# Performance work log

Measured on AMD Instinct MI355X. Metric: run time of the kernel, lower is better.

Reference implementation:

```python
import jax, jax.numpy as jnp
import numpy as np

H = 2048           # hidden size
IN_F = 64          # in_features
OUT_F = 3          # out_features
NEG_SLOPE = 0.01   # LeakyReLU default


def setup_inputs() -> dict:
    key = jax.random.key(0)
    ks = jax.random.split(key, 11)
    N = 32768
    return {
        "p": jax.random.normal(ks[0], (N, IN_F), dtype=jnp.float32),
        "init_w": jax.random.normal(ks[1], (H, IN_F), dtype=jnp.float32) * 0.05,
        "init_b": jax.random.normal(ks[2], (H,), dtype=jnp.float32) * 0.05,
        "w1": jax.random.normal(ks[3], (H, H), dtype=jnp.float32) * 0.02,
        "b1": jax.random.normal(ks[4], (H,), dtype=jnp.float32) * 0.02,
        "w2": jax.random.normal(ks[5], (H, H), dtype=jnp.float32) * 0.02,
        "b2": jax.random.normal(ks[6], (H,), dtype=jnp.float32) * 0.02,
        "w3": jax.random.normal(ks[7], (H, H), dtype=jnp.float32) * 0.02,
        "b3": jax.random.normal(ks[8], (H,), dtype=jnp.float32) * 0.02,
        "out_w": jax.random.normal(ks[9], (OUT_F, H), dtype=jnp.float32) * 0.05,
        "out_b": jax.random.normal(ks[10], (OUT_F,), dtype=jnp.float32) * 0.05,
    }


def _leaky_relu(x):
    return jnp.where(x > 0, x, NEG_SLOPE * x)


def reference(p, init_w, init_b, w1, b1, w2, b2, w3, b3, out_w, out_b):
    # eval mode: StructuredDropout with eval_size=None -> plain init linear
    flat = p.reshape(-1, p.shape[-1])                      # [N, IN_F]
    x = flat @ init_w.T + init_b                           # [N, H]
    # upper-triangular mask (in==out, backflow=0 -> diagonal=0)
    mask = jnp.triu(jnp.ones((H, H), dtype=bool))
    # hidden TriangleLinear layers; flip = (i % 2 == 1)
    for W, b, flip in ((w1, b1, False), (w2, b2, True), (w3, b3, False)):
        y = _leaky_relu(x) @ jnp.where(mask, W, 0.0).T + b  # [N, H]
        x = y[..., ::-1] if flip else y
    x = _leaky_relu(x)
    out = x @ out_w.T + out_b                              # [N, OUT_F]
    return out.reshape(p.shape[:-1] + (OUT_F,))
```

## Files before the change

kernel.cpp:

```cpp
#include <hip/hip_runtime.h>
#include <hip/hip_bf16.h>

#define NEG 0.01f

using f32x4  = __attribute__((ext_vector_type(4))) float;
using bf16x8 = __attribute__((ext_vector_type(8))) short;

__device__ __forceinline__ unsigned short f2b(float f) {
  union { float f; unsigned int u; } v; v.f = f;
  unsigned int r = (v.u + 0x7fffu + ((v.u >> 16) & 1u)) >> 16;
  return (unsigned short)r;
}
__device__ __forceinline__ float b2f(unsigned int bits) {
  union { unsigned int u; float f; } v; v.u = bits << 16;
  return v.f;
}

__device__ __forceinline__ void gload16(const unsigned short* g, unsigned short* l) {
  __builtin_amdgcn_global_load_lds(
      (const __attribute__((address_space(1))) unsigned int*)g,
      (__attribute__((address_space(3))) unsigned int*)l, 16, 0, 0);
}

__global__ void k_cvt(const float* __restrict__ in, unsigned short* __restrict__ out, int n4) {
  int i = blockIdx.x * blockDim.x + threadIdx.x;
  int stride = gridDim.x * blockDim.x;
  for (; i < n4; i += stride) {
    float4 v = reinterpret_cast<const float4*>(in)[i];
    ushort4 o;
    o.x = f2b(v.x); o.y = f2b(v.y); o.z = f2b(v.z); o.w = f2b(v.w);
    reinterpret_cast<ushort4*>(out)[i] = o;
  }
}

__global__ void k_cvt_tri(const float* __restrict__ W, unsigned short* __restrict__ out, int anti) {
  const int H = 2048;
  int i = blockIdx.x;
  const float* wr = W + (size_t)i * H;
  unsigned short* orow = out + (size_t)i * H;
  if (!anti) {
    for (int j = threadIdx.x; j < H; j += blockDim.x) {
      float v = (j >= i) ? wr[j] : 0.f;
      orow[j] = f2b(v);
    }
  } else {
    for (int k = threadIdx.x; k < H; k += blockDim.x) {
      int j = H - 1 - k;
      float v = (j >= i) ? wr[j] : 0.f;
      orow[k] = f2b(v);
    }
  }
}

__launch_bounds__(512)
__global__ void k_gemm(const unsigned short* __restrict__ A, int lda,
                       const unsigned short* __restrict__ B, int ldb,
                       const float* __restrict__ bias,
                       unsigned short* __restrict__ C, int ldc,
                       int K, int mode) {
  __shared__ unsigned short As[128 * 32];
  __shared__ unsigned short Bs[256 * 32];
  const int tid  = threadIdx.x;
  const int w    = tid >> 6;
  const int lane = tid & 63;

  const int nwg = gridDim.x;
  const int q   = nwg >> 3;
  const int L   = blockIdx.x;
  const int logical = (L & 7) * q + (L >> 3);
  const int bx = logical & 7;
  const int by = logical >> 3;
  const int brow = by * 128;
  const int bcol = bx * 256;

  int kstart = 0, kend = K;
  if (mode == 1) kstart = bcol;
  else if (mode == 2) kend = K - bcol;

  const int wm = w >> 2;
  const int wn = w & 3;
  f32x4 zero = {0.f, 0.f, 0.f, 0.f};
  f32x4 acc[4][4];
#pragma unroll
  for (int i = 0; i < 4; i++)
#pragma unroll
    for (int j = 0; j < 4; j++) acc[i][j] = zero;

  const int sr = lane >> 2;
  const int sc = (lane & 3) * 8;
  const unsigned short* Abase = A + (size_t)(brow + w * 16 + sr) * lda + sc;
  const unsigned short* Bbase = B + (size_t)(bcol + w * 16 + sr) * ldb + sc;
  unsigned short* AsW = &As[(w * 16) * 32];
  unsigned short* BsW = &Bs[(w * 16) * 32];

  const int lrow = lane & 15;
  const int lk   = (lane >> 4) * 8;

  for (int kt = kstart; kt < kend; kt += 32) {
    gload16(Abase + kt,                        AsW);
    gload16(Bbase + kt,                        BsW);
    gload16(Bbase + (size_t)128 * ldb + kt,    BsW + 128 * 32);
    __syncthreads();

    bf16x8 af[4], bfr[4];
#pragma unroll
    for (int i = 0; i < 4; i++) {
      af[i]  = *reinterpret_cast<const bf16x8*>(&As[(wm * 64 + i * 16 + lrow) * 32 + lk]);
      bfr[i] = *reinterpret_cast<const bf16x8*>(&Bs[(wn * 64 + i * 16 + lrow) * 32 + lk]);
    }
#pragma unroll
    for (int i = 0; i < 4; i++)
#pragma unroll
      for (int j = 0; j < 4; j++)
        acc[i][j] = __builtin_amdgcn_mfma_f32_16x16x32_bf16(af[i], bfr[j], acc[i][j], 0, 0, 0);
    __syncthreads();
  }

  const int orow0 = brow + wm * 64 + (lane >> 4) * 4;
  const int ocol0 = bcol + wn * 64 + (lane & 15);
#pragma unroll
  for (int j = 0; j < 4; j++) {
    int col = ocol0 + j * 16;
    float bv = bias[col];
#pragma unroll
    for (int i = 0; i < 4; i++) {
#pragma unroll
      for (int r = 0; r < 4; r++) {
        int row = orow0 + i * 16 + r;
        float v = acc[i][j][r] + bv;
        v = v > 0.f ? v : NEG * v;
        C[(size_t)row * ldc + col] = f2b(v);
      }
    }
  }
}

__global__ void k_out(const unsigned short* __restrict__ A,
                      const float* __restrict__ ow, const float* __restrict__ ob,
                      float* __restrict__ out) {
  const int H = 2048;
  int w = threadIdx.x >> 6, lane = threadIdx.x & 63;
  size_t n = (size_t)blockIdx.x * 4 + w;
  const unsigned short* a = A + n * H;
  float s0 = 0.f, s1 = 0.f, s2 = 0.f;
  for (int h0 = lane * 8; h0 < H; h0 += 512) {
    uint4 u = *reinterpret_cast<const uint4*>(&a[h0]);
    unsigned int uu[4] = {u.x, u.y, u.z, u.w};
#pragma unroll
    for (int q = 0; q < 4; q++) {
      int h = h0 + q * 2;
      float x0 = b2f(uu[q] & 0xffffu);
      float x1 = b2f(uu[q] >> 16);
      s0 += x0 * ow[h]         + x1 * ow[h + 1];
      s1 += x0 * ow[H + h]     + x1 * ow[H + h + 1];
      s2 += x0 * ow[2 * H + h] + x1 * ow[2 * H + h + 1];
    }
  }
#pragma unroll
  for (int off = 32; off > 0; off >>= 1) {
    s0 += __shfl_down(s0, off);
    s1 += __shfl_down(s1, off);
    s2 += __shfl_down(s2, off);
  }
  if (lane == 0) {
    out[n * 3 + 0] = s0 + ob[0];
    out[n * 3 + 1] = s1 + ob[1];
    out[n * 3 + 2] = s2 + ob[2];
  }
}

extern "C" void kernel_launch(void* const* d_in, const int* in_sizes, int n_in,
                              void* d_out, int out_size, void* d_ws, size_t ws_size,
                              hipStream_t stream) {
  const int N = 32768, H = 2048, INF_ = 64;
  const float* p      = (const float*)d_in[0];
  const float* init_w = (const float*)d_in[1];
  const float* init_b = (const float*)d_in[2];
  const float* w1     = (const float*)d_in[3];
  const float* b1     = (const float*)d_in[4];
  const float* w2     = (const float*)d_in[5];
  const float* b2     = (const float*)d_in[6];
  const float* w3     = (const float*)d_in[7];
  const float* b3     = (const float*)d_in[8];
  const float* ow     = (const float*)d_in[9];
  const float* ob     = (const float*)d_in[10];

  char* wsb = (char*)d_ws;
  size_t off = 0;
  auto alloc = [&](size_t bytes) -> char* {
    char* q = wsb + off;
    off += (bytes + 255) & ~(size_t)255;
    return q;
  };
  unsigned short* pb  = (unsigned short*)alloc((size_t)N * INF_ * 2);
  unsigned short* iwb = (unsigned short*)alloc((size_t)H * INF_ * 2);
  unsigned short* w1m = (unsigned short*)alloc((size_t)H * H * 2);
  unsigned short* w2m = (unsigned short*)alloc((size_t)H * H * 2);
  unsigned short* w3m = (unsigned short*)alloc((size_t)H * H * 2);

  size_t remain = (ws_size > off) ? (ws_size - off) : 0;
  long long ncll = (long long)(remain / ((size_t)H * 2 * 2));
  int Nc = (int)((ncll / 128) * 128);
  if (Nc > N) Nc = N;
  if (Nc < 128) return;

  unsigned short* bufA = (unsigned short*)(wsb + off);
  unsigned short* bufB = bufA + (size_t)Nc * H;

  k_cvt<<<2048, 256, 0, stream>>>(p, pb, N * INF_ / 4);
  k_cvt<<<32,   256, 0, stream>>>(init_w, iwb, H * INF_ / 4);
  k_cvt_tri<<<H, 256, 0, stream>>>(w1, w1m, 0);
  k_cvt_tri<<<H, 256, 0, stream>>>(w2, w2m, 0);
  k_cvt_tri<<<H, 256, 0, stream>>>(w3, w3m, 1);

  for (int n0 = 0; n0 < N; n0 += Nc) {
    int nc = (N - n0 < Nc) ? (N - n0) : Nc;
    int nblk = (H / 256) * (nc / 128);
    k_gemm<<<nblk, 512, 0, stream>>>(pb + (size_t)n0 * INF_, INF_, iwb, INF_, init_b,
                                     bufA, H, INF_, 0);
    k_gemm<<<nblk, 512, 0, stream>>>(bufA, H, w1m, H, b1, bufB, H, H, 1);
    k_gemm<<<nblk, 512, 0, stream>>>(bufB, H, w2m, H, b2, bufA, H, H, 1);
    k_gemm<<<nblk, 512, 0, stream>>>(bufA, H, w3m, H, b3, bufB, H, H, 2);
    k_out<<<nc / 4, 256, 0, stream>>>(bufB, ow, ob, (float*)d_out + (size_t)n0 * 3);
  }
}
```

Before: 859.5 us.

## Rewrite GEMM with 256x256 tiles, double-buffered LDS and swizzled layout

```diff
diff --git a/kernel.cpp b/kernel.cpp
--- a/kernel.cpp
+++ b/kernel.cpp
@@ -52,81 +52,125 @@
   }
 }
 
-__launch_bounds__(512)
-__global__ void k_gemm(const unsigned short* __restrict__ A, int lda,
-                       const unsigned short* __restrict__ B, int ldb,
-                       const float* __restrict__ bias,
-                       unsigned short* __restrict__ C, int ldc,
-                       int K, int mode) {
-  __shared__ unsigned short As[128 * 32];
-  __shared__ unsigned short Bs[256 * 32];
-  const int tid  = threadIdx.x;
-  const int w    = tid >> 6;
-  const int lane = tid & 63;
+__launch_bounds__(512, 2)
+__global__ void k_gemm8(const unsigned short* __restrict__ A, int lda,
+                        const unsigned short* __restrict__ B, int ldb,
+                        const float* __restrict__ bias,
+                        unsigned short* __restrict__ C, int ldc,
+                        int K, int mode) {
+  extern __shared__ unsigned short lds[];
+  const int tid = threadIdx.x;
+  const int w   = tid >> 6;
+  const int l   = tid & 63;
 
   const int nwg = gridDim.x;
-  const int q   = nwg >> 3;
+  const int q8  = nwg >> 3;
   const int L   = blockIdx.x;
-  const int logical = (L & 7) * q + (L >> 3);
-  const int bx = logical & 7;
+  const int logical = (L & 7) * q8 + (L >> 3);
   const int by = logical >> 3;
-  const int brow = by * 128;
+  const int bx = (logical + by) & 7;
+  const int brow = by * 256;
   const int bcol = bx * 256;
 
   int kstart = 0, kend = K;
   if (mode == 1) kstart = bcol;
   else if (mode == 2) kend = K - bcol;
+  const int nt = (kend - kstart) >> 6;
 
   const int wm = w >> 2;
   const int wn = w & 3;
-  f32x4 zero = {0.f, 0.f, 0.f, 0.f};
-  f32x4 acc[4][4];
-#pragma unroll
-  for (int i = 0; i < 4; i++)
-#pragma unroll
-    for (int j = 0; j < 4; j++) acc[i][j] = zero;
-
-  const int sr = lane >> 2;
-  const int sc = (lane & 3) * 8;
-  const unsigned short* Abase = A + (size_t)(brow + w * 16 + sr) * lda + sc;
-  const unsigned short* Bbase = B + (size_t)(bcol + w * 16 + sr) * ldb + sc;
-  unsigned short* AsW = &As[(w * 16) * 32];
-  unsigned short* BsW = &Bs[(w * 16) * 32];
-
-  const int lrow = lane & 15;
-  const int lk   = (lane >> 4) * 8;
-
-  for (int kt = kstart; kt < kend; kt += 32) {
-    gload16(Abase + kt,                        AsW);
-    gload16(Bbase + kt,                        BsW);
-    gload16(Bbase + (size_t)128 * ldb + kt,    BsW + 128 * 32);
-    __syncthreads();
-
-    bf16x8 af[4], bfr[4];
-#pragma unroll
-    for (int i = 0; i < 4; i++) {
-      af[i]  = *reinterpret_cast<const bf16x8*>(&As[(wm * 64 + i * 16 + lrow) * 32 + lk]);
-      bfr[i] = *reinterpret_cast<const bf16x8*>(&Bs[(wn * 64 + i * 16 + lrow) * 32 + lk]);
-    }
-#pragma unroll
-    for (int i = 0; i < 4; i++)
-#pragma unroll
-      for (int j = 0; j < 4; j++)
-        acc[i][j] = __builtin_amdgcn_mfma_f32_16x16x32_bf16(af[i], bfr[j], acc[i][j], 0, 0, 0);
-    __syncthreads();
-  }
-
-  const int orow0 = brow + wm * 64 + (lane >> 4) * 4;
-  const int ocol0 = bcol + wn * 64 + (lane & 15);
+
+  f32x4 acc[8][4];
+#pragma unroll
+  for (int i = 0; i < 8; i++)
+#pragma unroll
+    for (int j = 0; j < 4; j++) acc[i][j] = (f32x4){0.f, 0.f, 0.f, 0.f};
+
+  const int srow  = l >> 2;
+  const int sperm = ((l & 3) - ((l >> 3) & 3)) & 3;
+  const unsigned short* Asrc = A + (size_t)(brow + w * 16 + srow) * lda + sperm * 8;
+  const unsigned short* Bsrc = B + (size_t)(bcol + w * 16 + srow) * ldb + sperm * 8;
+  const int rdoff = (l & 15) * 64 + ((((l >> 4) + ((l >> 1) & 7)) & 3) << 4);
+
+  auto ldsAt = [&](int byteoff) -> unsigned short* {
+    return (unsigned short*)((char*)lds + byteoff);
+  };
+  auto stage_tile = [&](int tk, int bb) {
+    const int kc = kstart + (tk << 6);
+#pragma unroll
+    for (int half = 0; half < 2; half++) {
+#pragma unroll
+      for (int qq = 0; qq < 2; qq++) {
+        gload16(Asrc + (size_t)(half * 128) * lda + kc + qq * 32,
+                ldsAt(bb * 65536 + half * 16384 + (w * 2 + qq) * 1024));
+        gload16(Bsrc + (size_t)(half * 128) * ldb + kc + qq * 32,
+                ldsAt(bb * 65536 + 32768 + half * 16384 + (w * 2 + qq) * 1024));
+      }
+    }
+  };
+
+  stage_tile(0, 0);
+  if (nt > 1) stage_tile(1, 1);
+
+  const int AbaseW = wm * 16384;
+  const int BbaseW = 32768 + (wn >> 1) * 16384 + (wn & 1) * 8192;
+
+  for (int t = 0; t < nt; t++) {
+    const int bb = t & 1;
+    const int Ab = bb * 65536 + AbaseW;
+    const int Bb = bb * 65536 + BbaseW;
+    if (t + 1 < nt) asm volatile("s_waitcnt vmcnt(8)" ::: "memory");
+    else            asm volatile("s_waitcnt vmcnt(0)" ::: "memory");
+    __builtin_amdgcn_s_barrier();
+    asm volatile("" ::: "memory");
+
+    bf16x8 aR[4][2], bR[2][2];
+#pragma unroll
+    for (int Q = 0; Q < 4; Q++) {
+      const int mh = Q >> 1, nh = Q & 1;
+      if (nh == 0) {
+#pragma unroll
+        for (int ii = 0; ii < 4; ii++)
+#pragma unroll
+          for (int kk = 0; kk < 2; kk++)
+            aR[ii][kk] = *(const bf16x8*)((char*)lds + Ab + ((mh * 4 + ii) * 2 + kk) * 1024 + rdoff);
+      }
+#pragma unroll
+      for (int jj = 0; jj < 2; jj++)
+#pragma unroll
+        for (int kk = 0; kk < 2; kk++)
+          bR[jj][kk] = *(const bf16x8*)((char*)lds + Bb + ((nh * 2 + jj) * 2 + kk) * 1024 + rdoff);
+
+      __builtin_amdgcn_s_setprio(1);
+#pragma unroll
+      for (int ii = 0; ii < 4; ii++)
+#pragma unroll
+        for (int jj = 0; jj < 2; jj++) {
+          acc[mh * 4 + ii][nh * 2 + jj] = __builtin_amdgcn_mfma_f32_16x16x32_bf16(
+              aR[ii][0], bR[jj][0], acc[mh * 4 + ii][nh * 2 + jj], 0, 0, 0);
+          acc[mh * 4 + ii][nh * 2 + jj] = __builtin_amdgcn_mfma_f32_16x16x32_bf16(
+              aR[ii][1], bR[jj][1], acc[mh * 4 + ii][nh * 2 + jj], 0, 0, 0);
+        }
+      __builtin_amdgcn_s_setprio(0);
+      if (Q < 3) __builtin_amdgcn_s_barrier();
+    }
+    asm volatile("s_waitcnt lgkmcnt(0)" ::: "memory");
+    __builtin_amdgcn_s_barrier();
+    asm volatile("" ::: "memory");
+    if (t + 2 < nt) stage_tile(t + 2, bb);
+  }
+
+  const int orow0 = brow + wm * 128 + ((l >> 4) << 2);
+  const int ocol0 = bcol + wn * 64 + (l & 15);
 #pragma unroll
   for (int j = 0; j < 4; j++) {
-    int col = ocol0 + j * 16;
-    float bv = bias[col];
-#pragma unroll
-    for (int i = 0; i < 4; i++) {
+    const int col = ocol0 + j * 16;
+    const float bv = bias[col];
+#pragma unroll
+    for (int i = 0; i < 8; i++) {
 #pragma unroll
       for (int r = 0; r < 4; r++) {
-        int row = orow0 + i * 16 + r;
+        const int row = orow0 + i * 16 + r;
         float v = acc[i][j][r] + bv;
         v = v > 0.f ? v : NEG * v;
         C[(size_t)row * ldc + col] = f2b(v);
@@ -185,6 +229,9 @@
   const float* ow     = (const float*)d_in[9];
   const float* ob     = (const float*)d_in[10];
 
+  hipFuncSetAttribute((const void*)k_gemm8,
+                      hipFuncAttributeMaxDynamicSharedMemorySize, 131072);
+
   char* wsb = (char*)d_ws;
   size_t off = 0;
   auto alloc = [&](size_t bytes) -> char* {
@@ -200,9 +247,9 @@
 
   size_t remain = (ws_size > off) ? (ws_size - off) : 0;
   long long ncll = (long long)(remain / ((size_t)H * 2 * 2));
-  int Nc = (int)((ncll / 128) * 128);
+  int Nc = (int)((ncll / 256) * 256);
   if (Nc > N) Nc = N;
-  if (Nc < 128) return;
+  if (Nc < 256) return;
 
   unsigned short* bufA = (unsigned short*)(wsb + off);
   unsigned short* bufB = bufA + (size_t)Nc * H;
@@ -215,12 +262,12 @@
 
   for (int n0 = 0; n0 < N; n0 += Nc) {
     int nc = (N - n0 < Nc) ? (N - n0) : Nc;
-    int nblk = (H / 256) * (nc / 128);
-    k_gemm<<<nblk, 512, 0, stream>>>(pb + (size_t)n0 * INF_, INF_, iwb, INF_, init_b,
-                                     bufA, H, INF_, 0);
-    k_gemm<<<nblk, 512, 0, stream>>>(bufA, H, w1m, H, b1, bufB, H, H, 1);
-    k_gemm<<<nblk, 512, 0, stream>>>(bufB, H, w2m, H, b2, bufA, H, H, 1);
-    k_gemm<<<nblk, 512, 0, stream>>>(bufA, H, w3m, H, b3, bufB, H, H, 2);
+    int nblk = (nc / 256) * (H / 256);
+    k_gemm8<<<nblk, 512, 131072, stream>>>(pb + (size_t)n0 * INF_, INF_, iwb, INF_,
+                                           init_b, bufA, H, INF_, 0);
+    k_gemm8<<<nblk, 512, 131072, stream>>>(bufA, H, w1m, H, b1, bufB, H, H, 1);
+    k_gemm8<<<nblk, 512, 131072, stream>>>(bufB, H, w2m, H, b2, bufA, H, H, 1);
+    k_gemm8<<<nblk, 512, 131072, stream>>>(bufA, H, w3m, H, b3, bufB, H, H, 2);
     k_out<<<nc / 4, 256, 0, stream>>>(bufB, ow, ob, (float*)d_out + (size_t)n0 * 3);
   }
 }
```

After: 903.2 us. +5.1%, slower.
